# Optimization experiments

Measured on AMD Instinct MI355X. Metric: run time of the kernel, lower is better.

Reference implementation:

```python
import jax, jax.numpy as jnp
import numpy as np
import math

B, S, E, H = 2, 2048, 1024, 16
HD = E // H          # head_dim = 64
HX = 64              # helix_dim
P = HX // 2          # helix pairs = 32

def setup_inputs() -> dict:
    key = jax.random.key(0)
    ks = jax.random.split(key, 12)
    sc = 0.02
    return {
        "x":    jax.random.normal(ks[0], (B, S, E), dtype=jnp.float32),
        "Wq":   jax.random.normal(ks[1], (E, E), dtype=jnp.float32) * sc,
        "bq":   jnp.zeros((E,), dtype=jnp.float32),
        "Wk":   jax.random.normal(ks[2], (E, E), dtype=jnp.float32) * sc,
        "bk":   jnp.zeros((E,), dtype=jnp.float32),
        "Wv":   jax.random.normal(ks[3], (E, E), dtype=jnp.float32) * sc,
        "bv":   jnp.zeros((E,), dtype=jnp.float32),
        "Wo":   jax.random.normal(ks[4], (E, E), dtype=jnp.float32) * sc,
        "bo":   jnp.zeros((E,), dtype=jnp.float32),
        "Whel": jax.random.normal(ks[5], (H, HX, HD), dtype=jnp.float32) * sc,
        "bhel": jnp.zeros((H, HX), dtype=jnp.float32),
    }

def _l2norm(x, eps=1e-12):
    # torch F.normalize(p=2, dim=-1): x / max(||x||, eps)
    n = jnp.sqrt(jnp.sum(x * x, axis=-1, keepdims=True))
    return x / jnp.maximum(n, eps)

def _scramble(t):
    # faithful to torch: (B,S,2) -> transpose(1,2) -> reshape(B,S,2),
    # vectorized over (H,P): t is (B,H,P,S,2)
    b, h, p, s, _ = t.shape
    return jnp.swapaxes(t, -1, -2).reshape(b, h, p, s, 2)

def reference(x, Wq, bq, Wk, bk, Wv, bv, Wo, bo, Whel, bhel):
    b, s, e = x.shape
    h, hx, hd = Whel.shape
    p = hx // 2
    q = x @ Wq.T + bq
    k = x @ Wk.T + bk
    v = x @ Wv.T + bv
    qh = q.reshape(b, s, h, hd)
    kh = k.reshape(b, s, h, hd)
    # per-head helical projections: (B,S,H,HX)
    q_hel = jnp.einsum('bshd,hed->bshe', qh, Whel) + bhel
    k_hel = jnp.einsum('bshd,hed->bshe', kh, Whel) + bhel
    # split into 2D coords, normalize each pair: (B,H,P,S,2)
    qn = _l2norm(q_hel.reshape(b, s, h, p, 2)).transpose(0, 2, 3, 1, 4)
    kn = _l2norm(k_hel.reshape(b, s, h, p, 2)).transpose(0, 2, 3, 1, 4)
    qn = _scramble(qn)
    kn = _scramble(kn)
    # helical similarity averaged over pairs: (B,H,S,S)
    helical = jnp.einsum('bhpsc,bhptc->bhst', qn, kn) / p
    # standard scaled dot-product scores
    dot = jnp.einsum('bshd,bthd->bhst', qh, kh) / math.sqrt(hd)
    alpha = 0.5
    attn = jax.nn.softmax(alpha * dot + (1.0 - alpha) * helical, axis=-1)
    vh = v.reshape(b, s, h, hd)
    out = jnp.einsum('bhst,bthd->bshd', attn, vh).reshape(b, s, e)
    return out @ Wo.T + bo
```

## Files before the change

kernel.cpp:

```cpp
#include <hip/hip_runtime.h>
#include <hip/hip_bf16.h>


typedef unsigned short u16;
typedef unsigned int u32;
typedef __attribute__((ext_vector_type(8))) __bf16 bf16x8;
typedef __attribute__((ext_vector_type(4))) float f32x4;
typedef __attribute__((ext_vector_type(16))) float f32x16;

union BFrag { u32 u[4]; bf16x8 b; };

__device__ __forceinline__ u16 f2b(float f) {
  u32 u = __float_as_uint(f);
  u32 r = (u + 0x7fffu + ((u >> 16) & 1u)) >> 16;
  return (u16)r;
}
__device__ __forceinline__ float b2f(u16 h) {
  return __uint_as_float(((u32)h) << 16);
}

__device__ __forceinline__ f32x4 mfma16(bf16x8 a, bf16x8 b, f32x4 c) {
  return __builtin_amdgcn_mfma_f32_16x16x32_bf16(a, b, c, 0, 0, 0);
}
__device__ __forceinline__ f32x16 mfma32(bf16x8 a, bf16x8 b, f32x16 c) {
  return __builtin_amdgcn_mfma_f32_32x32x16_bf16(a, b, c, 0, 0, 0);
}

__device__ __forceinline__ void gld16(void* lds, const void* g) {
  __builtin_amdgcn_global_load_lds(
      (const __attribute__((address_space(1))) unsigned int*)g,
      (__attribute__((address_space(3))) unsigned int*)lds, 16, 0, 0);
}

__device__ __forceinline__ void pl32swap(u32& a, u32& b, int l5) {
#if __has_builtin(__builtin_amdgcn_permlane32_swap)
  typedef unsigned int u32x2v __attribute__((ext_vector_type(2)));
  u32x2v r = __builtin_amdgcn_permlane32_swap(a, b, false, false);
  a = r[0];
  b = r[1];
#else
  u32 ea = __shfl_xor((int)a, 32);
  u32 eb = __shfl_xor((int)b, 32);
  u32 na = l5 ? eb : a;
  u32 nb = l5 ? b : ea;
  a = na;
  b = nb;
#endif
}

#define LOG2E 1.4426950408889634f

__global__ __launch_bounds__(256) void cast_kernel(
    const float* __restrict__ x,  const float* __restrict__ wq,
    const float* __restrict__ wk, const float* __restrict__ wv,
    const float* __restrict__ wo, const float* __restrict__ whel,
    u16* __restrict__ xb, u16* __restrict__ wb, u16* __restrict__ wob,
    u16* __restrict__ whb) {
  long long q = (long long)blockIdx.x * 256 + threadIdx.x;
  const float* s; u16* d; long long base;
  if (q < 1048576)      { s = x;    d = xb;            base = 0; }
  else if (q < 1310720) { s = wq;   d = wb;            base = 1048576; }
  else if (q < 1572864) { s = wk;   d = wb + 1048576;  base = 1310720; }
  else if (q < 1835008) { s = wv;   d = wb + 2097152;  base = 1572864; }
  else if (q < 2097152) { s = wo;   d = wob;           base = 1835008; }
  else                  { s = whel; d = whb;           base = 2097152; }
  long long e = (q - base) * 4;
  float4 v = *(const float4*)(s + e);
  ushort4 o;
  o.x = f2b(v.x); o.y = f2b(v.y); o.z = f2b(v.z); o.w = f2b(v.w);
  *(ushort4*)(d + e) = o;
}

__global__ __launch_bounds__(256, 3) void qkv_gemm(
    const u16* __restrict__ xb, const u16* __restrict__ wb,
    const float* __restrict__ bq, const float* __restrict__ bk,
    const float* __restrict__ bv, const u16* __restrict__ whb,
    const float* __restrict__ bhel,
    u16* __restrict__ Qcat, u16* __restrict__ Kcat, u16* __restrict__ vt) {
  union SM {
    struct { u16 Al[2][128][32]; u16 Bl[2][128][32]; u16 T[64][136]; } m;
    struct { u16 Th[4][32][72]; u16 Hs[2][128][64]; } e;
  };
  __shared__ SM sm;
  const int nt = blockIdx.x, mt = blockIdx.y;
  const int which = nt >> 3;
  const int n0 = (nt & 7) << 7;
  const int m0 = mt << 7;
  const int tid = threadIdx.x;
  const int wave = tid >> 6, lane = tid & 63;
  const int g = lane >> 4, c15 = lane & 15;
  const int wm = wave & 1, wn = wave >> 1;
  const u16* Wp = wb + (long long)which * (1024 * 1024) + n0 * 1024;
  const u16* Ap = xb + m0 * 1024;
  const int srow = (wave * 64 + lane) >> 2;
  const int scol = (lane & 3) << 3;

  f32x4 acc[4][4];
#pragma unroll
  for (int i = 0; i < 4; i++)
#pragma unroll
    for (int j = 0; j < 4; j++) acc[i][j] = f32x4{0.f, 0.f, 0.f, 0.f};

  gld16(&sm.m.Al[0][srow][scol],      Ap + srow * 1024 + scol);
  gld16(&sm.m.Al[0][64 + srow][scol], Ap + (64 + srow) * 1024 + scol);
  gld16(&sm.m.Bl[0][srow][scol],      Wp + srow * 1024 + scol);
  gld16(&sm.m.Bl[0][64 + srow][scol], Wp + (64 + srow) * 1024 + scol);

  for (int k0 = 0; k0 < 1024; k0 += 32) {
    const int c = (k0 >> 5) & 1;
    __syncthreads();
    if (k0 + 32 < 1024) {
      const int kn = k0 + 32;
      gld16(&sm.m.Al[c ^ 1][srow][scol],      Ap + srow * 1024 + kn + scol);
      gld16(&sm.m.Al[c ^ 1][64 + srow][scol],
            Ap + (64 + srow) * 1024 + kn + scol);
      gld16(&sm.m.Bl[c ^ 1][srow][scol],      Wp + srow * 1024 + kn + scol);
      gld16(&sm.m.Bl[c ^ 1][64 + srow][scol],
            Wp + (64 + srow) * 1024 + kn + scol);
    }
    bf16x8 a[4], b[4];
#pragma unroll
    for (int i = 0; i < 4; i++)
      a[i] = *(const bf16x8*)&sm.m.Al[c][wm * 64 + i * 16 + c15][g * 8];
#pragma unroll
    for (int j = 0; j < 4; j++)
      b[j] = *(const bf16x8*)&sm.m.Bl[c][wn * 64 + j * 16 + c15][g * 8];
#pragma unroll
    for (int i = 0; i < 4; i++)
#pragma unroll
      for (int j = 0; j < 4; j++) acc[i][j] = mfma16(a[i], b[j], acc[i][j]);
  }

  if (which == 2) {
#pragma unroll
    for (int half = 0; half < 2; ++half) {
      __syncthreads();
      if (wn == half) {
#pragma unroll
        for (int i = 0; i < 4; i++)
#pragma unroll
          for (int j = 0; j < 4; j++)
#pragma unroll
            for (int r = 0; r < 4; r++) {
              int nloc = j * 16 + c15;
              int mloc = wm * 64 + i * 16 + g * 4 + r;
              float v = acc[i][j][r] + bv[n0 + half * 64 + nloc];
              sm.m.T[nloc][mloc] = f2b(v);
            }
      }
      __syncthreads();
#pragma unroll
      for (int it = 0; it < 4; ++it) {
        int idx = it * 256 + tid;
        int row = idx >> 4;
        int cm = (idx & 15) * 8;
        int col = n0 + half * 64 + row;
        int hh = col >> 6, dd = col & 63;
        int m = m0 + cm;
        int bb2 = m >> 11, s = m & 2047;
        *(uint4*)&vt[(((bb2 * 16 + hh) * 64) + dd) * 2048 + s] =
            *(const uint4*)&sm.m.T[row][cm];
      }
    }
    return;
  }

  const float* bias = (which == 0) ? bq : bk;
  const float fold = (which == 0) ? (0.0625f * LOG2E) : 1.0f;
  const float osc  = (which == 0) ? (0.125f * LOG2E) : 0.125f;
  const int h0 = n0 >> 6;
  const int hsel = h0 + wn;
  u16* Dst = ((which == 0) ? Qcat : Kcat);

  bf16x8 wf[2][4];
#pragma unroll
  for (int kh = 0; kh < 2; ++kh)
#pragma unroll
    for (int nf = 0; nf < 4; ++nf)
      wf[kh][nf] = *(const bf16x8*)(whb + hsel * 4096 + (nf * 16 + c15) * 64 +
                                    kh * 32 + g * 8);

  __syncthreads();
  const int bb2 = m0 >> 11;
  const int ubase = (m0 & 2047) >> 1;

#pragma unroll
  for (int half = 0; half < 2; ++half) {
#pragma unroll
    for (int i2 = 0; i2 < 2; ++i2) {
      int i = half * 2 + i2;
#pragma unroll
      for (int j = 0; j < 4; ++j)
#pragma unroll
        for (int r = 0; r < 4; ++r) {
          int row = m0 + wm * 64 + i * 16 + g * 4 + r;
          int col = n0 + wn * 64 + j * 16 + c15;
          float vraw = acc[i][j][r] + bias[col];
          int bb = row >> 11, s = row & 2047;
          int d = col & 63;
          Dst[(((long long)(bb * 16 + hsel) * 2048) + s) * 128 + d] =
              f2b(vraw * fold);
          sm.e.Th[wave][i2 * 16 + g * 4 + r][j * 16 + c15] = f2b(vraw);
        }
    }
    f32x4 hacc[2][4];
#pragma unroll
    for (int mf = 0; mf < 2; ++mf)
#pragma unroll
      for (int nf = 0; nf < 4; ++nf) hacc[mf][nf] = f32x4{0.f, 0.f, 0.f, 0.f};
#pragma unroll
    for (int kh = 0; kh < 2; ++kh) {
      bf16x8 a0 = *(const bf16x8*)&sm.e.Th[wave][c15][kh * 32 + g * 8];
      bf16x8 a1 = *(const bf16x8*)&sm.e.Th[wave][16 + c15][kh * 32 + g * 8];
#pragma unroll
      for (int nf = 0; nf < 4; ++nf) {
        hacc[0][nf] = mfma16(a0, wf[kh][nf], hacc[0][nf]);
        hacc[1][nf] = mfma16(a1, wf[kh][nf], hacc[1][nf]);
      }
    }
#pragma unroll
    for (int mf = 0; mf < 2; ++mf)
#pragma unroll
      for (int nf = 0; nf < 4; ++nf)
#pragma unroll
        for (int r = 0; r < 4; ++r) {
          int e = nf * 16 + c15;
          float v = hacc[mf][nf][r] + bhel[hsel * 64 + e];
          float pp = __shfl_xor(v, 1);
          float nn = sqrtf(v * v + pp * pp);
          float o = v / fmaxf(nn, 1e-12f) * osc;
          int tl = wm * 64 + half * 32 + mf * 16 + g * 4 + r;
          sm.e.Hs[wn][(e & 1) * 64 + (tl >> 1)][(e & ~1) | (tl & 1)] = f2b(o);
        }
  }
  __syncthreads();
#pragma unroll
  for (int it = 0; it < 8; ++it) {
    int idx = it * 256 + tid;
    int hh = idx >> 10;
    int hr = (idx >> 3) & 127;
    int ck = idx & 7;
    int coord = hr >> 6, ul = hr & 63;
    int row_out = coord * 1024 + ubase + ul;
    *(uint4*)&Dst[(((long long)(bb2 * 16 + h0 + hh) * 2048) + row_out) * 128 +
                  64 + ck * 8] = *(const uint4*)&sm.e.Hs[hh][hr][ck * 8];
  }
}

__global__ __launch_bounds__(512, 2) void attn_kernel(
    const u16* __restrict__ Qcat, const u16* __restrict__ Kcat,
    const u16* __restrict__ vt, u16* __restrict__ AO) {
  __shared__ u16 Kl[2][64][128];
  __shared__ u16 Vl[2][64][64];
  __shared__ float denl[2][256];
  const int bh = blockIdx.x, qt = blockIdx.y;
  const int bb = bh >> 4, h = bh & 15;
  const int q0 = qt << 8;
  const int tid = threadIdx.x;
  const int w = tid >> 6, lane = tid & 63;
  const int wq = w & 3, wt = w >> 2;
  const int l31 = lane & 31, l5 = lane >> 5;
  const u16* Qb = Qcat + (long long)bh * (2048 * 128);
  const u16* Kb = Kcat + (long long)bh * (2048 * 128);
  const u16* Vb = vt + (long long)bh * (64 * 2048);

  bf16x8 qf0[8], qf1[8];
  {
    const u16* qrow0 = Qb + (q0 + 64 * wq + l31) * 128 + l5 * 8;
    const u16* qrow1 = qrow0 + 32 * 128;
#pragma unroll
    for (int ks = 0; ks < 8; ++ks) {
      qf0[ks] = *(const bf16x8*)(qrow0 + ks * 16);
      qf1[ks] = *(const bf16x8*)(qrow1 + ks * 16);
    }
  }

  const int ll = tid;
  const int krow0 = ll >> 4;
  const int kp = ll & 15;
  const int ksrc0 = (kp & 8) | ((kp & 7) ^ (krow0 & 7));
  const int krow1 = 32 + krow0;
  const int ksrc1 = (kp & 8) | ((kp & 7) ^ (krow1 & 7));
  const int vd = ll >> 3;
  const int vsrc = (ll & 7) ^ (vd & 7);

  gld16(((u16*)Kl[0]) + ll * 8,        Kb + krow0 * 128 + ksrc0 * 8);
  gld16(((u16*)Kl[0]) + 4096 + ll * 8, Kb + krow1 * 128 + ksrc1 * 8);
  gld16(((u16*)Vl[0]) + ll * 8,        Vb + vd * 2048 + vsrc * 8);

  f32x16 accO00, accO01, accO10, accO11;
#pragma unroll
  for (int i = 0; i < 16; ++i) {
    accO00[i] = 0.f; accO01[i] = 0.f; accO10[i] = 0.f; accO11[i] = 0.f;
  }
  float den0 = 0.f, den1 = 0.f;

  const int krow = 32 * wt + l31;
  const int kr7 = krow & 7;

  for (int t = 0; t < 32; ++t) {
    const int cur = t & 1;
    __syncthreads();
    if (t + 1 < 32) {
      const int t1 = (t + 1) << 6;
      u16* Kd = (u16*)Kl[cur ^ 1];
      gld16(Kd + ll * 8,        Kb + (t1 + krow0) * 128 + ksrc0 * 8);
      gld16(Kd + 4096 + ll * 8, Kb + (t1 + krow1) * 128 + ksrc1 * 8);
      gld16(((u16*)Vl[cur ^ 1]) + ll * 8, Vb + vd * 2048 + t1 + vsrc * 8);
    }

    f32x16 accS0, accS1;
#pragma unroll
    for (int i = 0; i < 16; ++i) { accS0[i] = 0.f; accS1[i] = 0.f; }
#pragma unroll
    for (int ks = 0; ks < 8; ++ks) {
      int lc = 2 * ks + l5;
      int p = (lc & 8) | ((lc & 7) ^ kr7);
      bf16x8 ak = *(const bf16x8*)&Kl[cur][krow][p * 8];
      accS0 = mfma32(ak, qf0[ks], accS0);
      accS1 = mfma32(ak, qf1[ks], accS1);
    }

    BFrag A0q0, A1q0, A0q1, A1q1;
    {
      u32 D0[2], D1[2], D2[2], D3[2];
#pragma unroll
      for (int rr = 0; rr < 4; ++rr) {
        float p0 = __builtin_amdgcn_exp2f(accS0[4 * rr + 0]);
        float p1 = __builtin_amdgcn_exp2f(accS0[4 * rr + 1]);
        float p2 = __builtin_amdgcn_exp2f(accS0[4 * rr + 2]);
        float p3 = __builtin_amdgcn_exp2f(accS0[4 * rr + 3]);
        den0 += (p0 + p1) + (p2 + p3);
        u32 lo = __builtin_amdgcn_perm(__float_as_uint(p1),
                                       __float_as_uint(p0), 0x07060302u);
        u32 hi = __builtin_amdgcn_perm(__float_as_uint(p3),
                                       __float_as_uint(p2), 0x07060302u);
        if (rr == 0) { D0[0] = lo; D0[1] = hi; }
        else if (rr == 1) { D1[0] = lo; D1[1] = hi; }
        else if (rr == 2) { D2[0] = lo; D2[1] = hi; }
        else { D3[0] = lo; D3[1] = hi; }
      }
      A0q0.u[0] = D0[0]; A0q0.u[2] = D1[0]; pl32swap(A0q0.u[0], A0q0.u[2], l5);
      A0q0.u[1] = D0[1]; A0q0.u[3] = D1[1]; pl32swap(A0q0.u[1], A0q0.u[3], l5);
      A1q0.u[0] = D2[0]; A1q0.u[2] = D3[0]; pl32swap(A1q0.u[0], A1q0.u[2], l5);
      A1q0.u[1] = D2[1]; A1q0.u[3] = D3[1]; pl32swap(A1q0.u[1], A1q0.u[3], l5);
    }
    {
      u32 D0[2], D1[2], D2[2], D3[2];
#pragma unroll
      for (int rr = 0; rr < 4; ++rr) {
        float p0 = __builtin_amdgcn_exp2f(accS1[4 * rr + 0]);
        float p1 = __builtin_amdgcn_exp2f(accS1[4 * rr + 1]);
        float p2 = __builtin_amdgcn_exp2f(accS1[4 * rr + 2]);
        float p3 = __builtin_amdgcn_exp2f(accS1[4 * rr + 3]);
        den1 += (p0 + p1) + (p2 + p3);
        u32 lo = __builtin_amdgcn_perm(__float_as_uint(p1),
                                       __float_as_uint(p0), 0x07060302u);
        u32 hi = __builtin_amdgcn_perm(__float_as_uint(p3),
                                       __float_as_uint(p2), 0x07060302u);
        if (rr == 0) { D0[0] = lo; D0[1] = hi; }
        else if (rr == 1) { D1[0] = lo; D1[1] = hi; }
        else if (rr == 2) { D2[0] = lo; D2[1] = hi; }
        else { D3[0] = lo; D3[1] = hi; }
      }
      A0q1.u[0] = D0[0]; A0q1.u[2] = D1[0]; pl32swap(A0q1.u[0], A0q1.u[2], l5);
      A0q1.u[1] = D0[1]; A0q1.u[3] = D1[1]; pl32swap(A0q1.u[1], A0q1.u[3], l5);
      A1q1.u[0] = D2[0]; A1q1.u[2] = D3[0]; pl32swap(A1q1.u[0], A1q1.u[2], l5);
      A1q1.u[1] = D2[1]; A1q1.u[3] = D3[1]; pl32swap(A1q1.u[1], A1q1.u[3], l5);
    }

#pragma unroll
    for (int dq = 0; dq < 2; ++dq) {
      int d = 32 * dq + l31;
      int d7 = d & 7;
#pragma unroll
      for (int ks = 0; ks < 2; ++ks) {
        int lc = 4 * wt + 2 * ks + l5;
        bf16x8 bvf = *(const bf16x8*)&Vl[cur][d][((lc ^ d7) & 7) * 8];
        if (dq == 0) {
          accO00 = mfma32(ks ? A1q0.b : A0q0.b, bvf, accO00);
          accO10 = mfma32(ks ? A1q1.b : A0q1.b, bvf, accO10);
        } else {
          accO01 = mfma32(ks ? A1q0.b : A0q0.b, bvf, accO01);
          accO11 = mfma32(ks ? A1q1.b : A0q1.b, bvf, accO11);
        }
      }
    }
  }

  den0 += __shfl_xor(den0, 32);
  den1 += __shfl_xor(den1, 32);
  if (lane < 32) {
    denl[wt][64 * wq + lane] = den0;
    denl[wt][64 * wq + 32 + lane] = den1;
  }

  float* Ssc = (float*)Kl;
#pragma unroll
  for (int dq = 0; dq < 2; ++dq) {
    __syncthreads();
    if (wt == 1) {
#pragma unroll
      for (int qs = 0; qs < 2; ++qs)
#pragma unroll
        for (int r = 0; r < 16; ++r) {
          int qr = (r & 3) + 8 * (r >> 2) + 4 * l5;
          float v = dq ? (qs ? accO11[r] : accO01[r])
                       : (qs ? accO10[r] : accO00[r]);
          Ssc[(wq * 64 + qs * 32 + qr) * 32 + l31] = v;
        }
    }
    __syncthreads();
    if (wt == 0) {
#pragma unroll
      for (int qs = 0; qs < 2; ++qs)
#pragma unroll
        for (int r = 0; r < 16; ++r) {
          int qr = (r & 3) + 8 * (r >> 2) + 4 * l5;
          int ql = 64 * wq + 32 * qs + qr;
          float inv = 1.0f / (denl[0][ql] + denl[1][ql]);
          float mine = dq ? (qs ? accO11[r] : accO01[r])
                          : (qs ? accO10[r] : accO00[r]);
          float o = (mine + Ssc[(wq * 64 + qs * 32 + qr) * 32 + l31]) * inv;
          long long base = ((long long)(bb * 2048 + q0 + ql) * 1024) + h * 64;
          AO[base + 32 * dq + l31] = f2b(o);
        }
    }
  }
}

__global__ __launch_bounds__(256, 2) void out_gemm(
    const u16* __restrict__ AO, const u16* __restrict__ wob,
    const float* __restrict__ bo, float* __restrict__ out) {
  __shared__ u16 Al[2][128][32];
  __shared__ u16 Bl[2][64][32];
  const int n0 = blockIdx.x << 6;
  const int m0 = blockIdx.y << 7;
  const int tid = threadIdx.x;
  const int wave = tid >> 6, lane = tid & 63;
  const int g = lane >> 4, c15 = lane & 15;
  const int wm = wave & 1, wn = wave >> 1;
  const u16* Wp = wob + n0 * 1024;
  const u16* Ap = AO + m0 * 1024;
  const int srow = tid >> 2;
  const int scol = (tid & 3) << 3;

  f32x4 acc[4][2];
#pragma unroll
  for (int i = 0; i < 4; i++)
#pragma unroll
    for (int j = 0; j < 2; j++) acc[i][j] = f32x4{0.f, 0.f, 0.f, 0.f};

  gld16(&Al[0][srow][scol],      Ap + srow * 1024 + scol);
  gld16(&Al[0][64 + srow][scol], Ap + (64 + srow) * 1024 + scol);
  gld16(&Bl[0][srow][scol],      Wp + srow * 1024 + scol);

  for (int k0 = 0; k0 < 1024; k0 += 32) {
    const int c = (k0 >> 5) & 1;
    __syncthreads();
    if (k0 + 32 < 1024) {
      const int kn = k0 + 32;
      gld16(&Al[c ^ 1][srow][scol],      Ap + srow * 1024 + kn + scol);
      gld16(&Al[c ^ 1][64 + srow][scol], Ap + (64 + srow) * 1024 + kn + scol);
      gld16(&Bl[c ^ 1][srow][scol],      Wp + srow * 1024 + kn + scol);
    }
    bf16x8 a[4], b[2];
#pragma unroll
    for (int i = 0; i < 4; i++)
      a[i] = *(const bf16x8*)&Al[c][wm * 64 + i * 16 + c15][g * 8];
#pragma unroll
    for (int j = 0; j < 2; j++)
      b[j] = *(const bf16x8*)&Bl[c][wn * 32 + j * 16 + c15][g * 8];
#pragma unroll
    for (int i = 0; i < 4; i++)
#pragma unroll
      for (int j = 0; j < 2; j++) acc[i][j] = mfma16(a[i], b[j], acc[i][j]);
  }
#pragma unroll
  for (int i = 0; i < 4; i++)
#pragma unroll
    for (int j = 0; j < 2; j++)
#pragma unroll
      for (int r = 0; r < 4; r++) {
        int row = m0 + wm * 64 + i * 16 + g * 4 + r;
        int col = n0 + wn * 32 + j * 16 + c15;
        out[row * 1024 + col] = acc[i][j][r] + bo[col];
      }
}

extern "C" void kernel_launch(void* const* d_in, const int* in_sizes, int n_in,
                              void* d_out, int out_size, void* d_ws,
                              size_t ws_size, hipStream_t stream) {
  const float* x    = (const float*)d_in[0];
  const float* Wq   = (const float*)d_in[1];
  const float* bq   = (const float*)d_in[2];
  const float* Wk   = (const float*)d_in[3];
  const float* bk   = (const float*)d_in[4];
  const float* Wv   = (const float*)d_in[5];
  const float* bv   = (const float*)d_in[6];
  const float* Wo   = (const float*)d_in[7];
  const float* bo   = (const float*)d_in[8];
  const float* Whel = (const float*)d_in[9];
  const float* bhel = (const float*)d_in[10];
  float* out = (float*)d_out;

  char* ws = (char*)d_ws;
  u16* xb   = (u16*)(ws + 0);
  u16* wb   = (u16*)(ws + 8388608);
  u16* wob  = (u16*)(ws + 14680064);
  u16* whb  = (u16*)(ws + 16777216);
  u16* Qcat = (u16*)(ws + 16908288);
  u16* Kcat = (u16*)(ws + 33685504);
  u16* vt   = (u16*)(ws + 50462720);
  u16* AO   = (u16*)(ws + 58851328);

  cast_kernel<<<dim3(8256), dim3(256), 0, stream>>>(x, Wq, Wk, Wv, Wo, Whel,
                                                    xb, wb, wob, whb);
  qkv_gemm<<<dim3(24, 32), dim3(256), 0, stream>>>(xb, wb, bq, bk, bv, whb,
                                                   bhel, Qcat, Kcat, vt);
  attn_kernel<<<dim3(32, 8), dim3(512), 0, stream>>>(Qcat, Kcat, vt, AO);
  out_gemm<<<dim3(16, 32), dim3(256), 0, stream>>>(AO, wob, bo, out);
}
```

Before: 235.2 us.

## Triple-buffer K/V and GEMM tiles with partial vmcnt waits and MFMA priority

Converts the attention and output-GEMM loops from double to triple buffering in shared memory. Each iteration prefetches two tiles ahead and waits with s_waitcnt vmcnt(3) instead of a full drain, so one tile's loads stay in flight across the barrier. The MFMA sections are also wrapped in s_setprio to favour matrix issue. This raises LDS use per block (attn goes from about 50KB to about 74KB), which may limit the 2-blocks-per-CU occupancy target. It also relies on gld16 being a direct-to-LDS load that vmcnt tracks.

Measured after the change: 227.4 us. -3.3%, faster.

```diff
diff --git a/kernel.cpp b/kernel.cpp
--- a/kernel.cpp
+++ b/kernel.cpp
@@ -49,6 +49,14 @@
 }
 
 #define LOG2E 1.4426950408889634f
+
+#define PIPE_BARRIER(N)                                         \
+  do {                                                          \
+    __builtin_amdgcn_sched_barrier(0);                          \
+    asm volatile("s_waitcnt vmcnt(" #N ")" ::: "memory");       \
+    __builtin_amdgcn_s_barrier();                               \
+    __builtin_amdgcn_sched_barrier(0);                          \
+  } while (0)
 
 __global__ __launch_bounds__(256) void cast_kernel(
     const float* __restrict__ x,  const float* __restrict__ wq,
@@ -250,8 +258,8 @@
 __global__ __launch_bounds__(512, 2) void attn_kernel(
     const u16* __restrict__ Qcat, const u16* __restrict__ Kcat,
     const u16* __restrict__ vt, u16* __restrict__ AO) {
-  __shared__ u16 Kl[2][64][128];
-  __shared__ u16 Vl[2][64][64];
+  __shared__ u16 Kl[3][64][128];
+  __shared__ u16 Vl[3][64][64];
   __shared__ float denl[2][256];
   const int bh = blockIdx.x, qt = blockIdx.y;
   const int bb = bh >> 4, h = bh & 15;
@@ -287,6 +295,9 @@
   gld16(((u16*)Kl[0]) + ll * 8,        Kb + krow0 * 128 + ksrc0 * 8);
   gld16(((u16*)Kl[0]) + 4096 + ll * 8, Kb + krow1 * 128 + ksrc1 * 8);
   gld16(((u16*)Vl[0]) + ll * 8,        Vb + vd * 2048 + vsrc * 8);
+  gld16(((u16*)Kl[1]) + ll * 8,        Kb + (64 + krow0) * 128 + ksrc0 * 8);
+  gld16(((u16*)Kl[1]) + 4096 + ll * 8, Kb + (64 + krow1) * 128 + ksrc1 * 8);
+  gld16(((u16*)Vl[1]) + ll * 8,        Vb + vd * 2048 + 64 + vsrc * 8);
 
   f32x16 accO00, accO01, accO10, accO11;
 #pragma unroll
@@ -298,20 +309,22 @@
   const int krow = 32 * wt + l31;
   const int kr7 = krow & 7;
 
+  int cur = 0;
   for (int t = 0; t < 32; ++t) {
-    const int cur = t & 1;
-    __syncthreads();
-    if (t + 1 < 32) {
-      const int t1 = (t + 1) << 6;
-      u16* Kd = (u16*)Kl[cur ^ 1];
-      gld16(Kd + ll * 8,        Kb + (t1 + krow0) * 128 + ksrc0 * 8);
-      gld16(Kd + 4096 + ll * 8, Kb + (t1 + krow1) * 128 + ksrc1 * 8);
-      gld16(((u16*)Vl[cur ^ 1]) + ll * 8, Vb + vd * 2048 + t1 + vsrc * 8);
+    if (t < 31) { PIPE_BARRIER(3); } else { PIPE_BARRIER(0); }
+    if (t + 2 < 32) {
+      const int pf = (cur >= 1) ? cur - 1 : 2;
+      const int t2 = (t + 2) << 6;
+      u16* Kd = (u16*)Kl[pf];
+      gld16(Kd + ll * 8,        Kb + (t2 + krow0) * 128 + ksrc0 * 8);
+      gld16(Kd + 4096 + ll * 8, Kb + (t2 + krow1) * 128 + ksrc1 * 8);
+      gld16(((u16*)Vl[pf]) + ll * 8, Vb + vd * 2048 + t2 + vsrc * 8);
     }
 
     f32x16 accS0, accS1;
 #pragma unroll
     for (int i = 0; i < 16; ++i) { accS0[i] = 0.f; accS1[i] = 0.f; }
+    __builtin_amdgcn_s_setprio(1);
 #pragma unroll
     for (int ks = 0; ks < 8; ++ks) {
       int lc = 2 * ks + l5;
@@ -320,6 +333,7 @@
       accS0 = mfma32(ak, qf0[ks], accS0);
       accS1 = mfma32(ak, qf1[ks], accS1);
     }
+    __builtin_amdgcn_s_setprio(0);
 
     BFrag A0q0, A1q0, A0q1, A1q1;
     {
@@ -369,6 +383,7 @@
       A1q1.u[1] = D2[1]; A1q1.u[3] = D3[1]; pl32swap(A1q1.u[1], A1q1.u[3], l5);
     }
 
+    __builtin_amdgcn_s_setprio(1);
 #pragma unroll
     for (int dq = 0; dq < 2; ++dq) {
       int d = 32 * dq + l31;
@@ -386,6 +401,8 @@
         }
       }
     }
+    __builtin_amdgcn_s_setprio(0);
+    cur = (cur == 2) ? 0 : cur + 1;
   }
 
   den0 += __shfl_xor(den0, 32);
@@ -432,8 +449,8 @@
 __global__ __launch_bounds__(256, 2) void out_gemm(
     const u16* __restrict__ AO, const u16* __restrict__ wob,
     const float* __restrict__ bo, float* __restrict__ out) {
-  __shared__ u16 Al[2][128][32];
-  __shared__ u16 Bl[2][64][32];
+  __shared__ u16 Al[3][128][32];
+  __shared__ u16 Bl[3][64][32];
   const int n0 = blockIdx.x << 6;
   const int m0 = blockIdx.y << 7;
   const int tid = threadIdx.x;
@@ -454,27 +471,32 @@
   gld16(&Al[0][srow][scol],      Ap + srow * 1024 + scol);
   gld16(&Al[0][64 + srow][scol], Ap + (64 + srow) * 1024 + scol);
   gld16(&Bl[0][srow][scol],      Wp + srow * 1024 + scol);
-
-  for (int k0 = 0; k0 < 1024; k0 += 32) {
-    const int c = (k0 >> 5) & 1;
-    __syncthreads();
-    if (k0 + 32 < 1024) {
-      const int kn = k0 + 32;
-      gld16(&Al[c ^ 1][srow][scol],      Ap + srow * 1024 + kn + scol);
-      gld16(&Al[c ^ 1][64 + srow][scol], Ap + (64 + srow) * 1024 + kn + scol);
-      gld16(&Bl[c ^ 1][srow][scol],      Wp + srow * 1024 + kn + scol);
+  gld16(&Al[1][srow][scol],      Ap + srow * 1024 + 32 + scol);
+  gld16(&Al[1][64 + srow][scol], Ap + (64 + srow) * 1024 + 32 + scol);
+  gld16(&Bl[1][srow][scol],      Wp + srow * 1024 + 32 + scol);
+
+  int cur = 0;
+  for (int it = 0; it < 32; ++it) {
+    if (it < 31) { PIPE_BARRIER(3); } else { PIPE_BARRIER(0); }
+    if (it + 2 < 32) {
+      const int pf = (cur >= 1) ? cur - 1 : 2;
+      const int kn = (it + 2) << 5;
+      gld16(&Al[pf][srow][scol],      Ap + srow * 1024 + kn + scol);
+      gld16(&Al[pf][64 + srow][scol], Ap + (64 + srow) * 1024 + kn + scol);
+      gld16(&Bl[pf][srow][scol],      Wp + srow * 1024 + kn + scol);
     }
     bf16x8 a[4], b[2];
 #pragma unroll
     for (int i = 0; i < 4; i++)
-      a[i] = *(const bf16x8*)&Al[c][wm * 64 + i * 16 + c15][g * 8];
+      a[i] = *(const bf16x8*)&Al[cur][wm * 64 + i * 16 + c15][g * 8];
 #pragma unroll
     for (int j = 0; j < 2; j++)
-      b[j] = *(const bf16x8*)&Bl[c][wn * 32 + j * 16 + c15][g * 8];
+      b[j] = *(const bf16x8*)&Bl[cur][wn * 32 + j * 16 + c15][g * 8];
 #pragma unroll
     for (int i = 0; i < 4; i++)
 #pragma unroll
       for (int j = 0; j < 2; j++) acc[i][j] = mfma16(a[i], b[j], acc[i][j]);
+    cur = (cur == 2) ? 0 : cur + 1;
   }
 #pragma unroll
   for (int i = 0; i < 4; i++)
```
